# Kernel tuning notes

Measured on AMD Instinct MI355X. Metric: run time of the kernel, lower is better.

Reference implementation:

```python
import jax, jax.numpy as jnp
import numpy as np

N = 50000   # nodes
E = 800000  # edges
D = 64      # feature dim
C = 1.0     # curvature
MIN_NORM = 1e-15
BALL_EPS = 4e-3  # float32 projection epsilon (hgcn convention)


def _artanh(x):
    x = jnp.clip(x, -1.0 + 1e-7, 1.0 - 1e-7)
    return jnp.arctanh(x)


def _norm(x):
    return jnp.maximum(jnp.linalg.norm(x, axis=-1, keepdims=True), MIN_NORM)


def expmap0(u, c):
    # euclidean2poincare: tangent at origin -> ball
    sqrt_c = jnp.sqrt(c)
    u_norm = _norm(u)
    return jnp.tanh(sqrt_c * u_norm) * u / (sqrt_c * u_norm)


def logmap0(p, c):
    # poincare2euclidean: ball -> tangent at origin
    sqrt_c = jnp.sqrt(c)
    p_norm = _norm(p)
    return _artanh(sqrt_c * p_norm) * p / (sqrt_c * p_norm)


def proj(x, c):
    sqrt_c = jnp.sqrt(c)
    norm = _norm(x)
    maxnorm = (1.0 - BALL_EPS) / sqrt_c
    return jnp.where(norm > maxnorm, x / norm * maxnorm, x)


def mobius_matvec(m, x, c):
    # m: [out, in], x: [N, in]
    sqrt_c = jnp.sqrt(c)
    x_norm = _norm(x)                      # [N,1]
    mx = x @ m.T                           # [N,out]
    mx_norm = _norm(mx)                    # [N,1]
    res = jnp.tanh(mx_norm / x_norm * _artanh(sqrt_c * x_norm)) * mx / (mx_norm * sqrt_c)
    zero_mask = jnp.all(mx == 0.0, axis=-1, keepdims=True)
    return jnp.where(zero_mask, jnp.zeros_like(res), res)


def setup_inputs() -> dict:
    key = jax.random.key(0)
    k1, k2, k3, k4 = jax.random.split(key, 4)
    # node features: small norm so points lie well inside the unit ball
    x = jax.random.normal(k1, (N, D), dtype=jnp.float32) * 0.05
    # xavier_uniform-ish scale for the weight
    W = jax.random.normal(k2, (D, D), dtype=jnp.float32) * np.float32(np.sqrt(2.0 / D))
    edge_index = jax.random.randint(k3, (2, E), 0, N)
    edge_weight = jax.random.uniform(k4, (E,), dtype=jnp.float32)
    return {"x": x, "W": W, "edge_weight": edge_weight, "edge_index": edge_index}


def reference(x, W, edge_weight, edge_index):
    c = jnp.float32(C)
    # Linear (dropout=0, no bias): mobius matvec in the ball
    hidden = mobius_matvec(W, x, c)                       # [N,D] in ball
    # poincare2euclidean
    hidden_e = logmap0(hidden, c)                         # [N,D]
    # sparse adjacency aggregation: support = A @ hidden_e
    row, col = edge_index[0], edge_index[1]
    msgs = edge_weight[:, None] * hidden_e[col]           # [E,D]
    support = jax.ops.segment_sum(msgs, row, num_segments=N)  # [N,D]
    # euclidean2poincare
    support = expmap0(support, c)
    # HypAct: logmap0(c_in) -> relu -> expmap0(c_out) -> proj
    xt = jax.nn.relu(logmap0(support, c))
    out = proj(expmap0(xt, c), c)
    return out
```

## Files before the change

### kernel.cpp

```cpp
#include <hip/hip_runtime.h>
#include <hip/hip_bf16.h>
#include <math.h>

#define DD 64
#define BROWS 64
#define BSH 6
#define MAXB 1024
#define CAPB 1536
typedef unsigned long long u64;
typedef unsigned int u32;
typedef unsigned short u16;

__global__ __launch_bounds__(256) void hgcn_linear(const float* __restrict__ x,
                                                   const float* __restrict__ W,
                                                   __hip_bfloat16* __restrict__ he,
                                                   int* __restrict__ bcur,
                                                   int* __restrict__ nspill,
                                                   int n) {
  if (blockIdx.x == 0) {
    for (int i = threadIdx.x; i < MAXB; i += 256) bcur[i] = 0;
    if (threadIdx.x == 0) nspill[0] = 0;
  }
  __shared__ float Wl[64][68];
  __shared__ float xs[16][64];
  const int tid = threadIdx.x;
  for (int i = tid; i < 64 * 64; i += 256) Wl[i >> 6][i & 63] = W[i];
  const int wave = tid >> 6, lane = tid & 63;
  const int rbase = blockIdx.x * 16 + wave * 4;
  float xv[4];
  #pragma unroll
  for (int q = 0; q < 4; ++q) {
    const int row = rbase + q;
    xv[q] = (row < n) ? x[(size_t)row * DD + lane] : 0.f;
    xs[wave * 4 + q][lane] = xv[q];
  }
  __syncthreads();

  const int j0 = (lane >> 3) & 7;
  #pragma unroll
  for (int q = 0; q < 4; ++q) {
    const int row = rbase + q;
    if (row >= n) break;
    float nx2 = xv[q] * xv[q];
    #pragma unroll
    for (int m = 1; m < 64; m <<= 1) nx2 += __shfl_xor(nx2, m);
    const float nx = fmaxf(sqrtf(nx2), 1e-15f);
    const float s  = atanhf(fminf(nx, 1.f - 1e-7f)) / nx;
    float acc = 0.f;
    #pragma unroll
    for (int jj = 0; jj < 16; ++jj) {
      const int k = ((jj + j0) & 15) << 2;
      const float4 xk = *reinterpret_cast<const float4*>(&xs[wave * 4 + q][k]);
      const float4 wk = *reinterpret_cast<const float4*>(&Wl[lane][k]);
      acc = fmaf(xk.x, wk.x, acc);
      acc = fmaf(xk.y, wk.y, acc);
      acc = fmaf(xk.z, wk.z, acc);
      acc = fmaf(xk.w, wk.w, acc);
    }
    he[(size_t)row * DD + lane] = __float2bfloat16(acc * s);
  }
}

#define BINB 1024
#define BINC 6144
__global__ __launch_bounds__(1024) void hgcn_bin(const int* __restrict__ ei,
                                                 const float* __restrict__ ew,
                                                 int* __restrict__ bcur,
                                                 u64* __restrict__ stage,
                                                 u64* __restrict__ spill,
                                                 int* __restrict__ nspill,
                                                 int ne) {
  __shared__ int h[MAXB], cur[MAXB], gp[MAXB];
  const int tid = threadIdx.x;
  h[tid] = 0; cur[tid] = 0;
  __syncthreads();
  const int eb = blockIdx.x * BINC;
  const int m = min(BINC, ne - eb);
  for (int i = tid; i < m; i += BINB) atomicAdd(&h[ei[eb + i] >> BSH], 1);
  __syncthreads();
  gp[tid] = h[tid] ? atomicAdd(&bcur[tid], h[tid]) : 0;
  __syncthreads();
  for (int i = tid; i < m; i += BINB) {
    const int r = ei[eb + i];
    const int c = ei[ne + eb + i];
    const float w = ew[eb + i];
    const int b = r >> BSH;
    const int pos = gp[b] + atomicAdd(&cur[b], 1);
    if (pos < CAPB) {
      stage[(size_t)b * CAPB + pos] =
          ((u64)__float_as_uint(w) << 32) | ((u32)(r & (BROWS - 1)) << 16) | (u32)c;
    } else {
      const int sp = atomicAdd(nspill, 1);
      spill[sp] = ((u64)__float_as_uint(w) << 32) | ((u32)(r & 0xffff) << 16) | (u32)c;
    }
  }
}

__global__ __launch_bounds__(1024) void hgcn_bagg(const u16* __restrict__ he,
                                                  const u64* __restrict__ stage,
                                                  const int* __restrict__ bcur,
                                                  const u64* __restrict__ spill,
                                                  const int* __restrict__ nspill,
                                                  float* __restrict__ out, int n) {
  __shared__ u64 ed[CAPB];
  __shared__ int lh[BROWS + 1];
  __shared__ int lcur[BROWS];
  const int t = threadIdx.x;
  const int b = blockIdx.x;
  const u64* sb = stage + (size_t)b * CAPB;
  const int cnt = min(bcur[b], CAPB);

  if (t < BROWS) lcur[t] = 0;
  __syncthreads();
  for (int i = t; i < cnt; i += 1024)
    atomicAdd(&lcur[(int)((sb[i] >> 16) & (BROWS - 1))], 1);
  __syncthreads();
  if (t < 64) {
    const int v = lcur[t];
    int sc = v;
    #pragma unroll
    for (int d = 1; d < 64; d <<= 1) {
      const int u2 = __shfl_up(sc, d);
      if (t >= d) sc += u2;
    }
    lh[t] = sc - v;
    lcur[t] = sc - v;
    if (t == 63) lh[64] = sc;
  }
  __syncthreads();
  for (int i = t; i < cnt; i += 1024) {
    const u64 p = sb[i];
    const int rl = (int)((p >> 16) & (BROWS - 1));
    const int pos = atomicAdd(&lcur[rl], 1);
    ed[pos] = p;
  }
  __syncthreads();

  const int row = t >> 4;
  const int u = t & 15;
  const int s = u >> 3;
  const int l = u & 7;
  float a[8] = {0.f, 0.f, 0.f, 0.f, 0.f, 0.f, 0.f, 0.f};

  int j = lh[row] + s;
  const int je = lh[row + 1];
  uint4 q = {0, 0, 0, 0};
  float w = 0.f;
  if (j < je) {
    const u64 p = ed[j];
    w = __uint_as_float((u32)(p >> 32));
    q = reinterpret_cast<const uint4*>(he + ((size_t)(p & 0xffffu) << 6))[l];
  }
  while (j < je) {
    const uint4 qc = q;
    const float wc = w;
    const int jn = j + 2;
    if (jn < je) {
      const u64 p = ed[jn];
      w = __uint_as_float((u32)(p >> 32));
      q = reinterpret_cast<const uint4*>(he + ((size_t)(p & 0xffffu) << 6))[l];
    }
    a[0] = fmaf(wc, __uint_as_float(qc.x << 16), a[0]);
    a[1] = fmaf(wc, __uint_as_float(qc.x & 0xffff0000u), a[1]);
    a[2] = fmaf(wc, __uint_as_float(qc.y << 16), a[2]);
    a[3] = fmaf(wc, __uint_as_float(qc.y & 0xffff0000u), a[3]);
    a[4] = fmaf(wc, __uint_as_float(qc.z << 16), a[4]);
    a[5] = fmaf(wc, __uint_as_float(qc.z & 0xffff0000u), a[5]);
    a[6] = fmaf(wc, __uint_as_float(qc.w << 16), a[6]);
    a[7] = fmaf(wc, __uint_as_float(qc.w & 0xffff0000u), a[7]);
    j = jn;
  }

  const int ns = nspill[0];
  for (int sidx = 0; sidx < ns; ++sidx) {
    const u64 p = spill[sidx];
    const int grow = (int)((p >> 16) & 0xffffu);
    if ((grow >> BSH) != b) continue;
    if ((grow & (BROWS - 1)) != row || s != 0) continue;
    const float ww = __uint_as_float((u32)(p >> 32));
    const uint4 qq = reinterpret_cast<const uint4*>(he + ((size_t)(p & 0xffffu) << 6))[l];
    a[0] = fmaf(ww, __uint_as_float(qq.x << 16), a[0]);
    a[1] = fmaf(ww, __uint_as_float(qq.x & 0xffff0000u), a[1]);
    a[2] = fmaf(ww, __uint_as_float(qq.y << 16), a[2]);
    a[3] = fmaf(ww, __uint_as_float(qq.y & 0xffff0000u), a[3]);
    a[4] = fmaf(ww, __uint_as_float(qq.z << 16), a[4]);
    a[5] = fmaf(ww, __uint_as_float(qq.z & 0xffff0000u), a[5]);
    a[6] = fmaf(ww, __uint_as_float(qq.w << 16), a[6]);
    a[7] = fmaf(ww, __uint_as_float(qq.w & 0xffff0000u), a[7]);
  }

  #pragma unroll
  for (int k = 0; k < 8; ++k) a[k] += __shfl_xor(a[k], 8);

  float ss = 0.f;
  #pragma unroll
  for (int k = 0; k < 8; ++k) { a[k] = fmaxf(a[k], 0.f); ss = fmaf(a[k], a[k], ss); }
  ss += __shfl_xor(ss, 1); ss += __shfl_xor(ss, 2); ss += __shfl_xor(ss, 4);
  const float nu = fmaxf(sqrtf(ss), 1e-15f);
  const float th = tanhf(nu);
  const float maxn = 1.0f - 4e-3f;
  const float scale = (th > maxn) ? (maxn / nu) : (th / nu);
  const int grow = (b << BSH) + row;
  if (s == 0 && grow < n) {
    float4* op = reinterpret_cast<float4*>(out + (size_t)grow * DD + (size_t)l * 8);
    op[0] = float4{a[0] * scale, a[1] * scale, a[2] * scale, a[3] * scale};
    op[1] = float4{a[4] * scale, a[5] * scale, a[6] * scale, a[7] * scale};
  }
}

__global__ __launch_bounds__(256) void hgcn_linf32(const float* __restrict__ x,
                                                   const float* __restrict__ W,
                                                   float* __restrict__ he, int n) {
  __shared__ float Wl[64][68];
  __shared__ float xs[4][64];
  const int tid = threadIdx.x;
  for (int i = tid; i < 64 * 64; i += 256) Wl[i >> 6][i & 63] = W[i];
  const int wave = tid >> 6, lane = tid & 63;
  const int row = blockIdx.x * 4 + wave;
  float xv = 0.f;
  if (row < n) xv = x[row * DD + lane];
  xs[wave][lane] = xv;
  __syncthreads();
  if (row >= n) return;
  float nx2 = xv * xv;
  #pragma unroll
  for (int m = 1; m < 64; m <<= 1) nx2 += __shfl_xor(nx2, m);
  const float nx = fmaxf(sqrtf(nx2), 1e-15f);
  const float s = atanhf(fminf(nx, 1.f - 1e-7f)) / nx;
  const int j0 = (lane >> 3) & 7;
  float acc = 0.f;
  #pragma unroll
  for (int jj = 0; jj < 16; ++jj) {
    const int k = ((jj + j0) & 15) << 2;
    const float4 xk = *reinterpret_cast<const float4*>(&xs[wave][k]);
    const float4 wk = *reinterpret_cast<const float4*>(&Wl[lane][k]);
    acc = fmaf(xk.x, wk.x, acc); acc = fmaf(xk.y, wk.y, acc);
    acc = fmaf(xk.z, wk.z, acc); acc = fmaf(xk.w, wk.w, acc);
  }
  he[row * DD + lane] = acc * s;
}

__global__ __launch_bounds__(256) void hgcn_zero(float* __restrict__ p, int n4) {
  const int i = blockIdx.x * 256 + threadIdx.x;
  if (i < n4) reinterpret_cast<float4*>(p)[i] = float4{0.f, 0.f, 0.f, 0.f};
}

__global__ __launch_bounds__(256) void hgcn_scatter(const float* __restrict__ he,
                                                    const int* __restrict__ ei,
                                                    const float* __restrict__ ew,
                                                    float* __restrict__ sup, int ne) {
  const int t = blockIdx.x * 256 + threadIdx.x;
  const int e = t >> 4, l = t & 15;
  if (e >= ne) return;
  const int row = ei[e];
  const int col = ei[ne + e];
  const float w = ew[e];
  const float4 v = *reinterpret_cast<const float4*>(he + (size_t)col * DD + l * 4);
  float* dst = sup + (size_t)row * DD + l * 4;
  unsafeAtomicAdd(dst + 0, w * v.x);
  unsafeAtomicAdd(dst + 1, w * v.y);
  unsafeAtomicAdd(dst + 2, w * v.z);
  unsafeAtomicAdd(dst + 3, w * v.w);
}

__global__ __launch_bounds__(256) void hgcn_final(const float* __restrict__ sup,
                                                  float* __restrict__ out, int n) {
  const int t = blockIdx.x * 256 + threadIdx.x;
  const int r = t >> 4, l = t & 15;
  if (r >= n) return;
  float4 v = *reinterpret_cast<const float4*>(sup + (size_t)r * DD + l * 4);
  v.x = fmaxf(v.x, 0.f); v.y = fmaxf(v.y, 0.f);
  v.z = fmaxf(v.z, 0.f); v.w = fmaxf(v.w, 0.f);
  float p = v.x*v.x + v.y*v.y + v.z*v.z + v.w*v.w;
  p += __shfl_xor(p, 1); p += __shfl_xor(p, 2);
  p += __shfl_xor(p, 4); p += __shfl_xor(p, 8);
  const float nu = fmaxf(sqrtf(p), 1e-15f);
  const float th = tanhf(nu);
  float scale = th / nu;
  const float maxn = 1.0f - 4e-3f;
  if (th > maxn) scale = maxn / nu;
  float4 o = {v.x*scale, v.y*scale, v.z*scale, v.w*scale};
  *reinterpret_cast<float4*>(out + (size_t)r * DD + l * 4) = o;
}

extern "C" void kernel_launch(void* const* d_in, const int* in_sizes, int n_in,
                              void* d_out, int out_size, void* d_ws, size_t ws_size,
                              hipStream_t stream) {
  const float* x  = (const float*)d_in[0];
  const float* W  = (const float*)d_in[1];
  const float* ew = (const float*)d_in[2];
  const int*   ei = (const int*)d_in[3];
  const int n  = in_sizes[0] / DD;
  const int ne = in_sizes[2];
  const int nb = (n + BROWS - 1) / BROWS;

  size_t off_he    = 0;
  size_t off_stage = off_he + (((size_t)n * DD * 2 + 15) / 16) * 16;
  size_t off_spill = off_stage + (size_t)MAXB * CAPB * 8;
  size_t off_bcur  = off_spill + (size_t)ne * 8;
  size_t off_nsp   = off_bcur + MAXB * 4;
  size_t need      = off_nsp + 64;

  const size_t mean = (size_t)ne / (size_t)nb;
  size_t sig = 1;
  while (sig * sig < mean) ++sig;
  const bool capOK = mean + 8 * sig <= CAPB;

  if (ws_size >= need && n <= 65535 && nb <= MAXB && capOK) {
    __hip_bfloat16* he = (__hip_bfloat16*)((char*)d_ws + off_he);
    u64* stage  = (u64*)((char*)d_ws + off_stage);
    u64* spill  = (u64*)((char*)d_ws + off_spill);
    int* bcur   = (int*)((char*)d_ws + off_bcur);
    int* nspill = (int*)((char*)d_ws + off_nsp);
    float* out  = (float*)d_out;

    hipLaunchKernelGGL(hgcn_linear, dim3((n + 15) / 16),           dim3(256),  0, stream,
                       x, W, he, bcur, nspill, n);
    hipLaunchKernelGGL(hgcn_bin,    dim3((ne + BINC - 1) / BINC),  dim3(BINB), 0, stream,
                       ei, ew, bcur, stage, spill, nspill, ne);
    hipLaunchKernelGGL(hgcn_bagg,   dim3(nb),                      dim3(1024), 0, stream,
                       (const u16*)he, stage, bcur, spill, nspill, out, n);
  } else {
    float* he  = (float*)d_out;
    float* sup = (float*)d_ws;
    float* out = (float*)d_out;
    const int n4 = n * DD / 4;
    hipLaunchKernelGGL(hgcn_zero,    dim3((n4 + 255) / 256),       dim3(256), 0, stream, sup, n4);
    hipLaunchKernelGGL(hgcn_linf32,  dim3((n + 3) / 4),            dim3(256), 0, stream, x, W, he, n);
    hipLaunchKernelGGL(hgcn_scatter, dim3((ne * 16 + 255) / 256),  dim3(256), 0, stream, he, ei, ew, sup, ne);
    hipLaunchKernelGGL(hgcn_final,   dim3((n * 16 + 255) / 256),   dim3(256), 0, stream, sup, out, n);
  }
}
```

Before: 71.32 us.

## Merge linear and binning kernels into one launch; cache staged edges in LDS

The mobius linear transform and the edge-binning pass become a single kernel, with blocks split by blockIdx into binning blocks and linear blocks (now 1024 threads, 64 rows each), so the two independent stages run at the same time. Zeroing of the bin counters moves into a tiny separate kernel. The aggregation kernel now copies its staged edge bucket into shared memory once instead of reading global memory twice. The change trades one launch for another and adds LDS use in the aggregation kernel, which may reduce its occupancy.

```diff
diff --git a/kernel.cpp b/kernel.cpp
--- a/kernel.cpp
+++ b/kernel.cpp
@@ -7,91 +7,91 @@
 #define BSH 6
 #define MAXB 1024
 #define CAPB 1536
+#define BINB 1024
+#define BINC 6144
 typedef unsigned long long u64;
 typedef unsigned int u32;
 typedef unsigned short u16;
 
-__global__ __launch_bounds__(256) void hgcn_linear(const float* __restrict__ x,
-                                                   const float* __restrict__ W,
-                                                   __hip_bfloat16* __restrict__ he,
-                                                   int* __restrict__ bcur,
-                                                   int* __restrict__ nspill,
-                                                   int n) {
-  if (blockIdx.x == 0) {
-    for (int i = threadIdx.x; i < MAXB; i += 256) bcur[i] = 0;
-    if (threadIdx.x == 0) nspill[0] = 0;
-  }
-  __shared__ float Wl[64][68];
-  __shared__ float xs[16][64];
+__global__ __launch_bounds__(1024) void hgcn_zero0(int* __restrict__ bcur,
+                                                   int* __restrict__ nspill) {
+  const int i = threadIdx.x;
+  if (i < MAXB) bcur[i] = 0;
+  if (i == 0) nspill[0] = 0;
+}
+
+__global__ __launch_bounds__(1024) void hgcn_linbin(const float* __restrict__ x,
+                                                    const float* __restrict__ W,
+                                                    __hip_bfloat16* __restrict__ he,
+                                                    const int* __restrict__ ei,
+                                                    const float* __restrict__ ew,
+                                                    int* __restrict__ bcur,
+                                                    u64* __restrict__ stage,
+                                                    u64* __restrict__ spill,
+                                                    int* __restrict__ nspill,
+                                                    int n, int ne, int nbin) {
   const int tid = threadIdx.x;
-  for (int i = tid; i < 64 * 64; i += 256) Wl[i >> 6][i & 63] = W[i];
-  const int wave = tid >> 6, lane = tid & 63;
-  const int rbase = blockIdx.x * 16 + wave * 4;
-  float xv[4];
-  #pragma unroll
-  for (int q = 0; q < 4; ++q) {
-    const int row = rbase + q;
-    xv[q] = (row < n) ? x[(size_t)row * DD + lane] : 0.f;
-    xs[wave * 4 + q][lane] = xv[q];
-  }
-  __syncthreads();
-
-  const int j0 = (lane >> 3) & 7;
-  #pragma unroll
-  for (int q = 0; q < 4; ++q) {
-    const int row = rbase + q;
-    if (row >= n) break;
-    float nx2 = xv[q] * xv[q];
+  if ((int)blockIdx.x < nbin) {
+    __shared__ int h[MAXB], cur[MAXB], gp[MAXB];
+    h[tid] = 0; cur[tid] = 0;
+    __syncthreads();
+    const int eb = blockIdx.x * BINC;
+    const int m = min(BINC, ne - eb);
+    for (int i = tid; i < m; i += BINB) atomicAdd(&h[ei[eb + i] >> BSH], 1);
+    __syncthreads();
+    gp[tid] = h[tid] ? atomicAdd(&bcur[tid], h[tid]) : 0;
+    __syncthreads();
+    for (int i = tid; i < m; i += BINB) {
+      const int r = ei[eb + i];
+      const int c = ei[ne + eb + i];
+      const float w = ew[eb + i];
+      const int b = r >> BSH;
+      const int pos = gp[b] + atomicAdd(&cur[b], 1);
+      if (pos < CAPB) {
+        stage[(size_t)b * CAPB + pos] =
+            ((u64)__float_as_uint(w) << 32) | ((u32)(r & (BROWS - 1)) << 16) | (u32)c;
+      } else {
+        const int sp = atomicAdd(nspill, 1);
+        spill[sp] = ((u64)__float_as_uint(w) << 32) | ((u32)(r & 0xffff) << 16) | (u32)c;
+      }
+    }
+  } else {
+    __shared__ float Wl[64][68];
+    __shared__ float xs[64][64];
+    const int lb = blockIdx.x - nbin;
+    for (int i = tid; i < 64 * 64; i += 1024) Wl[i >> 6][i & 63] = W[i];
+    const int wave = tid >> 6, lane = tid & 63;
+    const int rbase = lb * 64 + wave * 4;
+    float xv[4];
     #pragma unroll
-    for (int m = 1; m < 64; m <<= 1) nx2 += __shfl_xor(nx2, m);
-    const float nx = fmaxf(sqrtf(nx2), 1e-15f);
-    const float s  = atanhf(fminf(nx, 1.f - 1e-7f)) / nx;
-    float acc = 0.f;
+    for (int q = 0; q < 4; ++q) {
+      const int row = rbase + q;
+      xv[q] = (row < n) ? x[(size_t)row * DD + lane] : 0.f;
+      xs[wave * 4 + q][lane] = xv[q];
+    }
+    __syncthreads();
+    const int j0 = (lane >> 3) & 7;
     #pragma unroll
-    for (int jj = 0; jj < 16; ++jj) {
-      const int k = ((jj + j0) & 15) << 2;
-      const float4 xk = *reinterpret_cast<const float4*>(&xs[wave * 4 + q][k]);
-      const float4 wk = *reinterpret_cast<const float4*>(&Wl[lane][k]);
-      acc = fmaf(xk.x, wk.x, acc);
-      acc = fmaf(xk.y, wk.y, acc);
-      acc = fmaf(xk.z, wk.z, acc);
-      acc = fmaf(xk.w, wk.w, acc);
-    }
-    he[(size_t)row * DD + lane] = __float2bfloat16(acc * s);
-  }
-}
-
-#define BINB 1024
-#define BINC 6144
-__global__ __launch_bounds__(1024) void hgcn_bin(const int* __restrict__ ei,
-                                                 const float* __restrict__ ew,
-                                                 int* __restrict__ bcur,
-                                                 u64* __restrict__ stage,
-                                                 u64* __restrict__ spill,
-                                                 int* __restrict__ nspill,
-                                                 int ne) {
-  __shared__ int h[MAXB], cur[MAXB], gp[MAXB];
-  const int tid = threadIdx.x;
-  h[tid] = 0; cur[tid] = 0;
-  __syncthreads();
-  const int eb = blockIdx.x * BINC;
-  const int m = min(BINC, ne - eb);
-  for (int i = tid; i < m; i += BINB) atomicAdd(&h[ei[eb + i] >> BSH], 1);
-  __syncthreads();
-  gp[tid] = h[tid] ? atomicAdd(&bcur[tid], h[tid]) : 0;
-  __syncthreads();
-  for (int i = tid; i < m; i += BINB) {
-    const int r = ei[eb + i];
-    const int c = ei[ne + eb + i];
-    const float w = ew[eb + i];
-    const int b = r >> BSH;
-    const int pos = gp[b] + atomicAdd(&cur[b], 1);
-    if (pos < CAPB) {
-      stage[(size_t)b * CAPB + pos] =
-          ((u64)__float_as_uint(w) << 32) | ((u32)(r & (BROWS - 1)) << 16) | (u32)c;
-    } else {
-      const int sp = atomicAdd(nspill, 1);
-      spill[sp] = ((u64)__float_as_uint(w) << 32) | ((u32)(r & 0xffff) << 16) | (u32)c;
+    for (int q = 0; q < 4; ++q) {
+      const int row = rbase + q;
+      if (row >= n) break;
+      float nx2 = xv[q] * xv[q];
+      #pragma unroll
+      for (int m = 1; m < 64; m <<= 1) nx2 += __shfl_xor(nx2, m);
+      const float nx = fmaxf(sqrtf(nx2), 1e-15f);
+      const float s  = atanhf(fminf(nx, 1.f - 1e-7f)) / nx;
+      float acc = 0.f;
+      #pragma unroll
+      for (int jj = 0; jj < 16; ++jj) {
+        const int k = ((jj + j0) & 15) << 2;
+        const float4 xk = *reinterpret_cast<const float4*>(&xs[wave * 4 + q][k]);
+        const float4 wk = *reinterpret_cast<const float4*>(&Wl[lane][k]);
+        acc = fmaf(xk.x, wk.x, acc);
+        acc = fmaf(xk.y, wk.y, acc);
+        acc = fmaf(xk.z, wk.z, acc);
+        acc = fmaf(xk.w, wk.w, acc);
+      }
+      he[(size_t)row * DD + lane] = __float2bfloat16(acc * s);
     }
   }
 }
@@ -102,6 +102,7 @@
                                                   const u64* __restrict__ spill,
                                                   const int* __restrict__ nspill,
                                                   float* __restrict__ out, int n) {
+  __shared__ u64 edr[CAPB];
   __shared__ u64 ed[CAPB];
   __shared__ int lh[BROWS + 1];
   __shared__ int lcur[BROWS];
@@ -110,10 +111,11 @@
   const u64* sb = stage + (size_t)b * CAPB;
   const int cnt = min(bcur[b], CAPB);
 
+  for (int i = t; i < cnt; i += 1024) edr[i] = sb[i];
   if (t < BROWS) lcur[t] = 0;
   __syncthreads();
   for (int i = t; i < cnt; i += 1024)
-    atomicAdd(&lcur[(int)((sb[i] >> 16) & (BROWS - 1))], 1);
+    atomicAdd(&lcur[(int)((edr[i] >> 16) & (BROWS - 1))], 1);
   __syncthreads();
   if (t < 64) {
     const int v = lcur[t];
@@ -129,7 +131,7 @@
   }
   __syncthreads();
   for (int i = t; i < cnt; i += 1024) {
-    const u64 p = sb[i];
+    const u64 p = edr[i];
     const int rl = (int)((p >> 16) & (BROWS - 1));
     const int pos = atomicAdd(&lcur[rl], 1);
     ed[pos] = p;
@@ -314,11 +316,13 @@
     int* nspill = (int*)((char*)d_ws + off_nsp);
     float* out  = (float*)d_out;
 
-    hipLaunchKernelGGL(hgcn_linear, dim3((n + 15) / 16),           dim3(256),  0, stream,
-                       x, W, he, bcur, nspill, n);
-    hipLaunchKernelGGL(hgcn_bin,    dim3((ne + BINC - 1) / BINC),  dim3(BINB), 0, stream,
-                       ei, ew, bcur, stage, spill, nspill, ne);
-    hipLaunchKernelGGL(hgcn_bagg,   dim3(nb),                      dim3(1024), 0, stream,
+    const int nbin = (ne + BINC - 1) / BINC;
+    const int nlin = (n + 63) / 64;
+
+    hipLaunchKernelGGL(hgcn_zero0,  dim3(1),           dim3(1024), 0, stream, bcur, nspill);
+    hipLaunchKernelGGL(hgcn_linbin, dim3(nbin + nlin), dim3(1024), 0, stream,
+                       x, W, he, ei, ew, bcur, stage, spill, nspill, n, ne, nbin);
+    hipLaunchKernelGGL(hgcn_bagg,   dim3(nb),          dim3(1024), 0, stream,
                        (const u16*)he, stage, bcur, spill, nspill, out, n);
   } else {
     float* he  = (float*)d_out;
```

Result: faster. 68.07 us (-4.6%).
